# Optimization experiments

Hardware: AMD Instinct MI355X
Metric: run time of the kernel (lower is better)

Reference implementation:

```python
import jax, jax.numpy as jnp
import numpy as np

N = 8192      # n_nodes (graphs[0].shape[0])
E = 262144    # n_edges (avg degree 32)
B = 16        # batch
T = 15        # time taps H of ChebTimeConv
K = 25        # Chebyshev order
G1, G2 = 32, 64
C, D = 512, 6


def setup_inputs() -> dict:
    key = jax.random.key(0)
    ks = jax.random.split(key, 8)
    x = jax.random.normal(ks[0], (B, N, T), jnp.float32)
    edge_index = jax.random.randint(ks[1], (2, E), 0, N, dtype=jnp.int64)
    # ChebTimeConv weights: K Chebyshev taps x T time taps (f_in=1) -> G1
    W1 = jax.random.normal(ks[2], (K, T, G1), jnp.float32) * 0.05
    b1 = jnp.zeros((G1,), jnp.float32)
    # ChebConv weights: K taps, G1 -> G2
    W2 = jax.random.normal(ks[3], (K, G1, G2), jnp.float32) * 0.05
    b2 = jnp.zeros((G2,), jnp.float32)
    fc1_w = jax.random.normal(ks[4], (C, N * G2), jnp.float32) * 0.01
    fc1_b = jnp.zeros((C,), jnp.float32)
    fc2_w = jax.random.normal(ks[5], (D, C), jnp.float32) * 0.05
    fc2_b = jnp.zeros((D,), jnp.float32)
    return dict(x=x, edge_index=edge_index, W1=W1, b1=b1, W2=W2, b2=b2,
                fc1_w=fc1_w, fc1_b=fc1_b, fc2_w=fc2_w, fc2_b=fc2_b)


def _cheb_edge_norm(edge_index, n):
    # PyG ChebConv normalization with lambda_max=2:
    # L_hat = 2L/lambda_max - I = -D^{-1/2} A D^{-1/2} (diag cancels to 0)
    row, col = edge_index[0], edge_index[1]
    deg = jnp.zeros((n,), jnp.float32).at[row].add(1.0)
    dinv = jnp.where(deg > 0, jax.lax.rsqrt(jnp.maximum(deg, 1.0)), 0.0)
    return -(dinv[row] * dinv[col])


def _cheb_conv(x, edge_index, W, b):
    # x: [B, N, Fin]; W: [K, Fin, Fout] -> [B, N, Fout]
    row, col = edge_index[0], edge_index[1]
    norm = _cheb_edge_norm(edge_index, x.shape[1])

    def Lhat(z):  # sparse L_hat @ z : gather at source row, scatter-add at col
        msg = z[:, row, :] * norm[None, :, None]
        return jnp.zeros_like(z).at[:, col, :].add(msg)

    Tx0 = x
    out = jnp.einsum('bnf,fg->bng', Tx0, W[0])
    Tx1 = Lhat(x)
    out = out + jnp.einsum('bnf,fg->bng', Tx1, W[1])
    for k in range(2, W.shape[0]):  # fixed small K=25 recursion
        Tx2 = 2.0 * Lhat(Tx1) - Tx0
        out = out + jnp.einsum('bnf,fg->bng', Tx2, W[k])
        Tx0, Tx1 = Tx1, Tx2
    return out + b


def reference(x, edge_index, W1, b1, W2, b2, fc1_w, fc1_b, fc2_w, fc2_b):
    # torch: real part of FFT over the time axis
    xf = jnp.fft.fft(x, axis=2).real.astype(x.dtype)          # [B, N, T]
    h = jax.nn.relu(_cheb_conv(xf, edge_index, W1, b1))       # [B, N, G1]
    h = jax.nn.relu(_cheb_conv(h, edge_index, W2, b2))        # [B, N, G2]
    h = h.reshape(h.shape[0], -1)                             # [B, N*G2]
    h = h @ fc1_w.T + fc1_b                                   # [B, C]
    h = h @ fc2_w.T + fc2_b                                   # [B, D]
    return jax.nn.log_softmax(h, axis=1)
```

## Files before the change

kernel.cpp:

```cpp
#include <hip/hip_runtime.h>
#include <hip/hip_bf16.h>

typedef _Float16 f16x2 __attribute__((ext_vector_type(2)));
typedef _Float16 f16x4 __attribute__((ext_vector_type(4)));
typedef _Float16 f16x8 __attribute__((ext_vector_type(8)));
typedef float f32x4 __attribute__((ext_vector_type(4)));

static constexpr int NNODE = 8192;
static constexpr int NEDGE = 262144;
static constexpr int NBATCH = 16;
static constexpr int TDIM = 15;
static constexpr int G1D = 32;
static constexpr int G2D = 64;
static constexpr int NK = 25;
static constexpr size_t NG2 = (size_t)NNODE * G2D;
static constexpr size_t ROWDW = 128;
static constexpr size_t SLICE = (size_t)NNODE * ROWDW;


__global__ void deg_cnt_kernel(const int* __restrict__ ei, int* __restrict__ deg,
                               int* __restrict__ cnt) {
    int e = blockIdx.x * 256 + threadIdx.x;
    if (e < NEDGE) {
        atomicAdd(&deg[ei[e]], 1);
        atomicAdd(&cnt[ei[NEDGE + e]], 1);
    }
}

__global__ void dinv_kernel(const int* __restrict__ deg, float* __restrict__ dinv) {
    int n = blockIdx.x * 256 + threadIdx.x;
    if (n < NNODE) dinv[n] = (deg[n] > 0) ? rsqrtf((float)deg[n]) : 0.f;
}

__global__ __launch_bounds__(1024) void scan_kernel(const int* __restrict__ cnt,
                                                    int* __restrict__ ptr) {
    __shared__ int s[1024];
    int t = threadIdx.x;
    int base = t * 8;
    int loc[8];
    int sum = 0;
#pragma unroll
    for (int i = 0; i < 8; ++i) { loc[i] = sum; sum += cnt[base + i]; }
    s[t] = sum;
    __syncthreads();
    for (int off = 1; off < 1024; off <<= 1) {
        int v = (t >= off) ? s[t - off] : 0;
        __syncthreads();
        s[t] += v;
        __syncthreads();
    }
    int prev = (t > 0) ? s[t - 1] : 0;
#pragma unroll
    for (int i = 0; i < 8; ++i) ptr[base + i] = prev + loc[i];
    if (t == 1023) ptr[NNODE] = s[1023];
}

__global__ void fill_kernel(const int* __restrict__ ei, const int* __restrict__ ptr,
                            int* __restrict__ fill, const float* __restrict__ dinv,
                            int* __restrict__ csr_src, float* __restrict__ csr_w) {
    int e = blockIdx.x * 256 + threadIdx.x;
    if (e < NEDGE) {
        int r = ei[e], c = ei[NEDGE + e];
        int pos = ptr[c] + atomicAdd(&fill[c], 1);
        csr_src[pos] = r;
        csr_w[pos] = -dinv[r] * dinv[c];
    }
}


__global__ __launch_bounds__(256) void fft_kernel(const float* __restrict__ x,
                                                  _Float16* __restrict__ T0) {
    int n = blockIdx.x;
    __shared__ float xl[NBATCH][TDIM];
    __shared__ float ct[TDIM][TDIM];
    int t = threadIdx.x;
    if (t < NBATCH * TDIM) {
        int b = t / TDIM, s = t % TDIM;
        xl[b][s] = x[((size_t)b * NNODE + n) * TDIM + s];
    }
    if (t < TDIM * TDIM) {
        int tt = t / TDIM, s = t % TDIM;
        ct[tt][s] = cosf(6.283185307179586f * (float)((tt * s) % TDIM) / 15.0f);
    }
    __syncthreads();
    int b = t >> 4, f = t & 15;
    float a = 0.f;
    if (f < TDIM) {
#pragma unroll
        for (int s = 0; s < TDIM; ++s) a += xl[b][s] * ct[f][s];
    }
    T0[(size_t)n * 256 + t] = (_Float16)a;
}


__global__ void wt_kernel(const float* __restrict__ W, _Float16* __restrict__ Wt,
                          int F, int G, int total) {
    int i = blockIdx.x * 256 + threadIdx.x;
    if (i < total) {
        int f = i & 31;
        int g = (i >> 5) % G;
        int k = i / (32 * G);
        float v = (f < F) ? W[((size_t)k * F + f) * G + g] : 0.f;
        Wt[i] = (_Float16)v;
    }
}


template <bool FIRST>
__global__ __launch_bounds__(128) void gather_step(
    const f16x2* __restrict__ Tsrc, const f16x2* __restrict__ T0,
    f16x2* __restrict__ T2, const int* __restrict__ cptr,
    const int* __restrict__ csrc, const float* __restrict__ cw) {
    __shared__ int es[128];
    __shared__ float ews[128];
    const int c = blockIdx.x;
    const int tid = threadIdx.x;

    float a0 = 0.f, a1 = 0.f;
    const int p0 = cptr[c], p1 = cptr[c + 1];
    for (int tb = p0; tb < p1; tb += 128) {
        int m = p1 - tb;
        if (m > 128) m = 128;
        __syncthreads();
        if (tid < m) { es[tid] = csrc[tb + tid]; ews[tid] = cw[tb + tid]; }
        __syncthreads();
        int j = 0;
        for (; j + 4 <= m; j += 4) {
            int s0 = es[j], s1 = es[j + 1], s2 = es[j + 2], s3 = es[j + 3];
            float w0 = ews[j], w1 = ews[j + 1], w2 = ews[j + 2], w3 = ews[j + 3];
            f16x2 r0 = Tsrc[(size_t)s0 * ROWDW + tid];
            f16x2 r1 = Tsrc[(size_t)s1 * ROWDW + tid];
            f16x2 r2 = Tsrc[(size_t)s2 * ROWDW + tid];
            f16x2 r3 = Tsrc[(size_t)s3 * ROWDW + tid];
            a0 += w0 * (float)r0[0]; a1 += w0 * (float)r0[1];
            a0 += w1 * (float)r1[0]; a1 += w1 * (float)r1[1];
            a0 += w2 * (float)r2[0]; a1 += w2 * (float)r2[1];
            a0 += w3 * (float)r3[0]; a1 += w3 * (float)r3[1];
        }
        for (; j < m; ++j) {
            int s = es[j]; float w = ews[j];
            f16x2 r = Tsrc[(size_t)s * ROWDW + tid];
            a0 += w * (float)r[0]; a1 += w * (float)r[1];
        }
    }

    f16x2 o;
    if (FIRST) {
        o[0] = (_Float16)a0; o[1] = (_Float16)a1;
    } else {
        f16x2 t0v = T0[(size_t)c * ROWDW + tid];
        o[0] = (_Float16)(2.f * a0 - (float)t0v[0]);
        o[1] = (_Float16)(2.f * a1 - (float)t0v[1]);
    }
    T2[(size_t)c * ROWDW + tid] = o;
}


template <int FDW, int G, int MODE>
__global__ __launch_bounds__(G * 4) void proj_kernel(
    const unsigned int* __restrict__ Tall, const _Float16* __restrict__ Wt,
    const float* __restrict__ bias, _Float16* __restrict__ dest) {
    constexpr int STRIDE = NK * 32 + 8;
    constexpr int NT = G * 4;
    __shared__ _Float16 A[16 * STRIDE];
    unsigned int* Adw = reinterpret_cast<unsigned int*>(A);

    const int n = blockIdx.x;
    const int tid = threadIdx.x;

    for (int i = tid; i < 16 * STRIDE / 2; i += NT) Adw[i] = 0u;
    __syncthreads();

    for (int idx = tid; idx < NK * 16 * FDW; idx += NT) {
        int k = idx / (16 * FDW);
        int r = idx % (16 * FDW);
        int b = r / FDW;
        int jp = r % FDW;
        size_t src;
        if (MODE == 0) {
            src = (size_t)k * SLICE + (size_t)n * ROWDW + b * FDW + jp;
        } else {
            src = (size_t)(k * 2 + (b >> 3)) * SLICE + (size_t)n * ROWDW + (b & 7) * FDW + jp;
        }
        Adw[b * (STRIDE / 2) + k * 16 + jp] = Tall[src];
    }
    __syncthreads();

    const int wv = tid >> 6, lane = tid & 63;
    const int m0 = lane & 15;
    const int krow = lane >> 4;
    const int k0 = krow * 8;
    const int g = wv * 16 + m0;

    const float bb = bias[g];
    f32x4 d = (f32x4){bb, bb, bb, bb};
#pragma unroll
    for (int k = 0; k < NK; ++k) {
        f16x8 af = *reinterpret_cast<const f16x8*>(&A[m0 * STRIDE + k * 32 + k0]);
        f16x8 bf = *reinterpret_cast<const f16x8*>(&Wt[((size_t)k * G + g) * 32 + k0]);
        d = __builtin_amdgcn_mfma_f32_16x16x32_f16(af, bf, d, 0, 0, 0);
    }
#pragma unroll
    for (int r = 0; r < 4; ++r) {
        int b = krow * 4 + r;
        _Float16 v = (_Float16)fmaxf(d[r], 0.f);
        if (MODE == 0) {
            dest[((size_t)(b >> 3) * NNODE + n) * 256 + (b & 7) * 32 + g] = v;
        } else {
            dest[(size_t)b * NG2 + (size_t)n * G2D + g] = v;
        }
    }
}


__global__ __launch_bounds__(512) void fc1_kernel(const _Float16* __restrict__ Hflat,
                                                  const float* __restrict__ fc1w,
                                                  float* __restrict__ partial) {
    int wave = threadIdx.x >> 6, lane = threadIdx.x & 63;
    int chunk = blockIdx.x & 127, cg = blockIdx.x >> 7;
    int c0 = (cg * 8 + wave) * 2;
    const float* w0 = fc1w + (size_t)c0 * NG2 + (size_t)chunk * 4096;
    const float* w1 = w0 + NG2;
    const _Float16* h = Hflat + (size_t)chunk * 4096;
    float a0[16], a1[16];
#pragma unroll
    for (int b = 0; b < 16; ++b) { a0[b] = 0.f; a1[b] = 0.f; }
    for (int it = 0; it < 16; ++it) {
        int j = it * 256 + lane * 4;
        float4 wv0 = *reinterpret_cast<const float4*>(w0 + j);
        float4 wv1 = *reinterpret_cast<const float4*>(w1 + j);
#pragma unroll
        for (int b = 0; b < 16; ++b) {
            f16x4 hv = *reinterpret_cast<const f16x4*>(h + (size_t)b * NG2 + j);
            float h0 = (float)hv[0], h1 = (float)hv[1], h2 = (float)hv[2], h3 = (float)hv[3];
            a0[b] += wv0.x * h0 + wv0.y * h1 + wv0.z * h2 + wv0.w * h3;
            a1[b] += wv1.x * h0 + wv1.y * h1 + wv1.z * h2 + wv1.w * h3;
        }
    }
#pragma unroll
    for (int b = 0; b < 16; ++b) {
        float v0 = a0[b], v1 = a1[b];
        for (int off = 32; off; off >>= 1) {
            v0 += __shfl_down(v0, off);
            v1 += __shfl_down(v1, off);
        }
        if (lane == 0) {
            partial[((size_t)chunk * 512 + c0) * 16 + b] = v0;
            partial[((size_t)chunk * 512 + c0 + 1) * 16 + b] = v1;
        }
    }
}

__global__ void fc1_reduce_kernel(const float* __restrict__ partial,
                                  const float* __restrict__ fc1b, float* __restrict__ h1) {
    int i = blockIdx.x * 256 + threadIdx.x;
    if (i < 512 * 16) {
        int b = i & 15, c = i >> 4;
        float s = fc1b[c];
        for (int ch = 0; ch < 128; ++ch) s += partial[((size_t)ch * 512 + c) * 16 + b];
        h1[b * 512 + c] = s;
    }
}

__global__ __launch_bounds__(1024) void fc2_kernel(const float* __restrict__ h1,
                                                   const float* __restrict__ fc2w,
                                                   const float* __restrict__ fc2b,
                                                   float* __restrict__ out) {
    __shared__ float z[16][8];
    int wave = threadIdx.x >> 6, lane = threadIdx.x & 63;
    for (int d = 0; d < 6; ++d) {
        float acc = 0.f;
        for (int c = lane; c < 512; c += 64) acc += h1[wave * 512 + c] * fc2w[d * 512 + c];
        for (int off = 32; off; off >>= 1) acc += __shfl_down(acc, off);
        if (lane == 0) z[wave][d] = acc + fc2b[d];
    }
    __syncthreads();
    int t = threadIdx.x;
    if (t < 96) {
        int b = t / 6, d = t % 6;
        float m = z[b][0];
#pragma unroll
        for (int j = 1; j < 6; ++j) m = fmaxf(m, z[b][j]);
        float se = 0.f;
#pragma unroll
        for (int j = 0; j < 6; ++j) se += expf(z[b][j] - m);
        out[b * 6 + d] = z[b][d] - m - logf(se);
    }
}


extern "C" void kernel_launch(void* const* d_in, const int* in_sizes, int n_in,
                              void* d_out, int out_size, void* d_ws, size_t ws_size,
                              hipStream_t stream) {
    const float* x = (const float*)d_in[0];
    const int* ei = (const int*)d_in[1];
    const float* W1 = (const float*)d_in[2];
    const float* b1 = (const float*)d_in[3];
    const float* W2 = (const float*)d_in[4];
    const float* b2 = (const float*)d_in[5];
    const float* fc1w = (const float*)d_in[6];
    const float* fc1b = (const float*)d_in[7];
    const float* fc2w = (const float*)d_in[8];
    const float* fc2b = (const float*)d_in[9];
    float* out = (float*)d_out;

    char* ws = (char*)d_ws;
    size_t o = 0;
    auto alloc = [&](size_t bytes) -> void* {
        void* p = ws + o;
        o += (bytes + 255) & ~(size_t)255;
        return p;
    };
    f16x2* Tall1 = (f16x2*)alloc(NK * SLICE * 4);
    f16x2* Tall2 = (f16x2*)alloc(NK * 2 * SLICE * 4);
    _Float16* Hflat = (_Float16*)alloc(NBATCH * NG2 * 2);
    float* partial = (float*)alloc((size_t)128 * 512 * 16 * 4);
    int* deg = (int*)alloc(3 * NNODE * 4);
    int* cnt = deg + NNODE;
    int* fill = cnt + NNODE;
    int* cptr = (int*)alloc((NNODE + 8) * 4);
    float* dinv = (float*)alloc(NNODE * 4);
    int* csr_src = (int*)alloc((size_t)NEDGE * 4);
    float* csr_w = (float*)alloc((size_t)NEDGE * 4);
    _Float16* Wt1 = (_Float16*)alloc(NK * G1D * 32 * 2);
    _Float16* Wt2 = (_Float16*)alloc(NK * G2D * 32 * 2);
    float* h1 = (float*)alloc(16 * 512 * 4);

    hipMemsetAsync(deg, 0, 3 * NNODE * 4, stream);
    deg_cnt_kernel<<<NEDGE / 256, 256, 0, stream>>>(ei, deg, cnt);
    dinv_kernel<<<NNODE / 256, 256, 0, stream>>>(deg, dinv);
    scan_kernel<<<1, 1024, 0, stream>>>(cnt, cptr);
    fill_kernel<<<NEDGE / 256, 256, 0, stream>>>(ei, cptr, fill, dinv, csr_src, csr_w);
    fft_kernel<<<NNODE, 256, 0, stream>>>(x, (_Float16*)Tall1);
    wt_kernel<<<(NK * G1D * 32 + 255) / 256, 256, 0, stream>>>(W1, Wt1, 15, G1D,
                                                               NK * G1D * 32);
    wt_kernel<<<(NK * G2D * 32 + 255) / 256, 256, 0, stream>>>(W2, Wt2, 32, G2D,
                                                               NK * G2D * 32);

    gather_step<true><<<NNODE, 128, 0, stream>>>(Tall1, nullptr, Tall1 + SLICE, cptr,
                                                 csr_src, csr_w);
    for (int k = 2; k < NK; ++k) {
        gather_step<false><<<NNODE, 128, 0, stream>>>(
            Tall1 + (size_t)(k - 1) * SLICE, Tall1 + (size_t)(k - 2) * SLICE,
            Tall1 + (size_t)k * SLICE, cptr, csr_src, csr_w);
    }
    proj_kernel<8, G1D, 0><<<NNODE, G1D * 4, 0, stream>>>(
        (const unsigned int*)Tall1, Wt1, b1, (_Float16*)Tall2);

    for (int h = 0; h < 2; ++h) {
        gather_step<true><<<NNODE, 128, 0, stream>>>(
            Tall2 + (size_t)h * SLICE, nullptr, Tall2 + (size_t)(2 + h) * SLICE, cptr,
            csr_src, csr_w);
        for (int k = 2; k < NK; ++k) {
            gather_step<false><<<NNODE, 128, 0, stream>>>(
                Tall2 + (size_t)((k - 1) * 2 + h) * SLICE,
                Tall2 + (size_t)((k - 2) * 2 + h) * SLICE,
                Tall2 + (size_t)(k * 2 + h) * SLICE, cptr, csr_src, csr_w);
        }
    }
    proj_kernel<16, G2D, 1><<<NNODE, G2D * 4, 0, stream>>>(
        (const unsigned int*)Tall2, Wt2, b2, Hflat);

    fc1_kernel<<<128 * 32, 512, 0, stream>>>(Hflat, fc1w, partial);
    fc1_reduce_kernel<<<32, 256, 0, stream>>>(partial, fc1b, h1);
    fc2_kernel<<<1, 1024, 0, stream>>>(h1, fc2w, fc2b, out);
}
```

Baseline: 1.687 ms.

## Split feature slices into 256B rows with XCD-aware wave-per-node gather

Splits each Chebyshev slice into narrower 64-dword sub-slices (two for layer 1, four for layer 2) and remaps block IDs so each XCD handles one sub-slice. That sub-slice's working set can then stay in that XCD's L2 during the gather. Each wave now processes one node, and edge indices and weights are broadcast with readlane instead of shared memory and syncthreads. The second layer's two half-batch loops are merged into one launch per step. The projection kernels are rewritten for the new layout, which adds index-mapping complexity.

```diff
diff --git a/kernel.cpp b/kernel.cpp
--- a/kernel.cpp
+++ b/kernel.cpp
@@ -14,8 +14,8 @@
 static constexpr int G2D = 64;
 static constexpr int NK = 25;
 static constexpr size_t NG2 = (size_t)NNODE * G2D;
-static constexpr size_t ROWDW = 128;
-static constexpr size_t SLICE = (size_t)NNODE * ROWDW;
+static constexpr size_t SROW = 64;
+static constexpr size_t SLICE = (size_t)NNODE * SROW;
 
 
 __global__ void deg_cnt_kernel(const int* __restrict__ ei, int* __restrict__ deg,
@@ -89,7 +89,7 @@
 #pragma unroll
         for (int s = 0; s < TDIM; ++s) a += xl[b][s] * ct[f][s];
     }
-    T0[(size_t)n * 256 + t] = (_Float16)a;
+    T0[((size_t)(b >> 3) * NNODE + n) * 128 + (b & 7) * 16 + f] = (_Float16)a;
 }
 
 
@@ -106,41 +106,52 @@
 }
 
 
-template <bool FIRST>
-__global__ __launch_bounds__(128) void gather_step(
-    const f16x2* __restrict__ Tsrc, const f16x2* __restrict__ T0,
-    f16x2* __restrict__ T2, const int* __restrict__ cptr,
+template <int Q, bool FIRST>
+__global__ __launch_bounds__(256, 8) void gather_step(
+    const f16x2* __restrict__ Tsrc, const f16x2* __restrict__ Tprev0,
+    f16x2* __restrict__ Tdst, const int* __restrict__ cptr,
     const int* __restrict__ csrc, const float* __restrict__ cw) {
-    __shared__ int es[128];
-    __shared__ float ews[128];
-    const int c = blockIdx.x;
-    const int tid = threadIdx.x;
-
+    constexpr int CH = 8 / Q;
+    const int bid = blockIdx.x;
+    const int xcd = bid & 7;
+    const int s = xcd / CH;
+    const int chunk = xcd % CH;
+    const int wv = threadIdx.x >> 6, lane = threadIdx.x & 63;
+    const int node = (chunk * (256 * Q) + (bid >> 3)) * 4 + wv;
+
+    const f16x2* __restrict__ src = Tsrc + (size_t)s * SLICE;
     float a0 = 0.f, a1 = 0.f;
-    const int p0 = cptr[c], p1 = cptr[c + 1];
-    for (int tb = p0; tb < p1; tb += 128) {
+    const int p0 = cptr[node], p1 = cptr[node + 1];
+    for (int tb = p0; tb < p1; tb += 64) {
         int m = p1 - tb;
-        if (m > 128) m = 128;
-        __syncthreads();
-        if (tid < m) { es[tid] = csrc[tb + tid]; ews[tid] = cw[tb + tid]; }
-        __syncthreads();
+        if (m > 64) m = 64;
+        const bool ok = lane < m;
+        int esrc = ok ? csrc[tb + lane] : 0;
+        unsigned int ewu = ok ? __float_as_uint(cw[tb + lane]) : 0u;
         int j = 0;
         for (; j + 4 <= m; j += 4) {
-            int s0 = es[j], s1 = es[j + 1], s2 = es[j + 2], s3 = es[j + 3];
-            float w0 = ews[j], w1 = ews[j + 1], w2 = ews[j + 2], w3 = ews[j + 3];
-            f16x2 r0 = Tsrc[(size_t)s0 * ROWDW + tid];
-            f16x2 r1 = Tsrc[(size_t)s1 * ROWDW + tid];
-            f16x2 r2 = Tsrc[(size_t)s2 * ROWDW + tid];
-            f16x2 r3 = Tsrc[(size_t)s3 * ROWDW + tid];
+            int s0 = __builtin_amdgcn_readlane(esrc, j);
+            int s1 = __builtin_amdgcn_readlane(esrc, j + 1);
+            int s2 = __builtin_amdgcn_readlane(esrc, j + 2);
+            int s3 = __builtin_amdgcn_readlane(esrc, j + 3);
+            float w0 = __uint_as_float(__builtin_amdgcn_readlane(ewu, j));
+            float w1 = __uint_as_float(__builtin_amdgcn_readlane(ewu, j + 1));
+            float w2 = __uint_as_float(__builtin_amdgcn_readlane(ewu, j + 2));
+            float w3 = __uint_as_float(__builtin_amdgcn_readlane(ewu, j + 3));
+            f16x2 r0 = src[(size_t)s0 * SROW + lane];
+            f16x2 r1 = src[(size_t)s1 * SROW + lane];
+            f16x2 r2 = src[(size_t)s2 * SROW + lane];
+            f16x2 r3 = src[(size_t)s3 * SROW + lane];
             a0 += w0 * (float)r0[0]; a1 += w0 * (float)r0[1];
             a0 += w1 * (float)r1[0]; a1 += w1 * (float)r1[1];
             a0 += w2 * (float)r2[0]; a1 += w2 * (float)r2[1];
             a0 += w3 * (float)r3[0]; a1 += w3 * (float)r3[1];
         }
         for (; j < m; ++j) {
-            int s = es[j]; float w = ews[j];
-            f16x2 r = Tsrc[(size_t)s * ROWDW + tid];
-            a0 += w * (float)r[0]; a1 += w * (float)r[1];
+            int sj = __builtin_amdgcn_readlane(esrc, j);
+            float wj = __uint_as_float(__builtin_amdgcn_readlane(ewu, j));
+            f16x2 r = src[(size_t)sj * SROW + lane];
+            a0 += wj * (float)r[0]; a1 += wj * (float)r[1];
         }
     }
 
@@ -148,41 +159,32 @@
     if (FIRST) {
         o[0] = (_Float16)a0; o[1] = (_Float16)a1;
     } else {
-        f16x2 t0v = T0[(size_t)c * ROWDW + tid];
-        o[0] = (_Float16)(2.f * a0 - (float)t0v[0]);
-        o[1] = (_Float16)(2.f * a1 - (float)t0v[1]);
-    }
-    T2[(size_t)c * ROWDW + tid] = o;
-}
-
-
-template <int FDW, int G, int MODE>
-__global__ __launch_bounds__(G * 4) void proj_kernel(
+        f16x2 t0 = (Tprev0 + (size_t)s * SLICE)[(size_t)node * SROW + lane];
+        o[0] = (_Float16)(2.f * a0 - (float)t0[0]);
+        o[1] = (_Float16)(2.f * a1 - (float)t0[1]);
+    }
+    (Tdst + (size_t)s * SLICE)[(size_t)node * SROW + lane] = o;
+}
+
+
+__global__ __launch_bounds__(128) void proj1_kernel(
     const unsigned int* __restrict__ Tall, const _Float16* __restrict__ Wt,
     const float* __restrict__ bias, _Float16* __restrict__ dest) {
     constexpr int STRIDE = NK * 32 + 8;
-    constexpr int NT = G * 4;
     __shared__ _Float16 A[16 * STRIDE];
     unsigned int* Adw = reinterpret_cast<unsigned int*>(A);
-
     const int n = blockIdx.x;
     const int tid = threadIdx.x;
 
-    for (int i = tid; i < 16 * STRIDE / 2; i += NT) Adw[i] = 0u;
-    __syncthreads();
-
-    for (int idx = tid; idx < NK * 16 * FDW; idx += NT) {
-        int k = idx / (16 * FDW);
-        int r = idx % (16 * FDW);
-        int b = r / FDW;
-        int jp = r % FDW;
-        size_t src;
-        if (MODE == 0) {
-            src = (size_t)k * SLICE + (size_t)n * ROWDW + b * FDW + jp;
-        } else {
-            src = (size_t)(k * 2 + (b >> 3)) * SLICE + (size_t)n * ROWDW + (b & 7) * FDW + jp;
-        }
-        Adw[b * (STRIDE / 2) + k * 16 + jp] = Tall[src];
+    for (int i = tid; i < 16 * STRIDE / 2; i += 128) Adw[i] = 0u;
+    __syncthreads();
+    for (int idx = tid; idx < NK * 128; idx += 128) {
+        int k = idx >> 7, r = idx & 127;
+        int h = r >> 6, j = r & 63;
+        int bl = j >> 3, jp = j & 7;
+        int b = h * 8 + bl;
+        Adw[b * (STRIDE / 2) + k * 16 + jp] =
+            Tall[((size_t)(k * 2 + h) * NNODE + n) * 64 + j];
     }
     __syncthreads();
 
@@ -191,24 +193,62 @@
     const int krow = lane >> 4;
     const int k0 = krow * 8;
     const int g = wv * 16 + m0;
-
     const float bb = bias[g];
     f32x4 d = (f32x4){bb, bb, bb, bb};
 #pragma unroll
     for (int k = 0; k < NK; ++k) {
         f16x8 af = *reinterpret_cast<const f16x8*>(&A[m0 * STRIDE + k * 32 + k0]);
-        f16x8 bf = *reinterpret_cast<const f16x8*>(&Wt[((size_t)k * G + g) * 32 + k0]);
+        f16x8 bf = *reinterpret_cast<const f16x8*>(&Wt[((size_t)k * G1D + g) * 32 + k0]);
         d = __builtin_amdgcn_mfma_f32_16x16x32_f16(af, bf, d, 0, 0, 0);
     }
 #pragma unroll
     for (int r = 0; r < 4; ++r) {
         int b = krow * 4 + r;
         _Float16 v = (_Float16)fmaxf(d[r], 0.f);
-        if (MODE == 0) {
-            dest[((size_t)(b >> 3) * NNODE + n) * 256 + (b & 7) * 32 + g] = v;
-        } else {
-            dest[(size_t)b * NG2 + (size_t)n * G2D + g] = v;
-        }
+        dest[((size_t)(b >> 2) * NNODE + n) * 128 + (b & 3) * 32 + g] = v;
+    }
+}
+
+
+__global__ __launch_bounds__(256) void proj2_kernel(
+    const unsigned int* __restrict__ Tall, const _Float16* __restrict__ Wt,
+    const float* __restrict__ bias, _Float16* __restrict__ dest) {
+    constexpr int STRIDE = NK * 32 + 8;
+    __shared__ _Float16 A[16 * STRIDE];
+    unsigned int* Adw = reinterpret_cast<unsigned int*>(A);
+    const int n = blockIdx.x;
+    const int tid = threadIdx.x;
+
+    for (int i = tid; i < 16 * STRIDE / 2; i += 256) Adw[i] = 0u;
+    __syncthreads();
+    for (int idx = tid; idx < NK * 256; idx += 256) {
+        int k = idx >> 8, r = idx & 255;
+        int q = r >> 6, j = r & 63;
+        int bl2 = j >> 4, jp = j & 15;
+        int b = q * 4 + bl2;
+        Adw[b * (STRIDE / 2) + k * 16 + jp] =
+            Tall[((size_t)(k * 4 + q) * NNODE + n) * 64 + j];
+    }
+    __syncthreads();
+
+    const int wv = tid >> 6, lane = tid & 63;
+    const int m0 = lane & 15;
+    const int krow = lane >> 4;
+    const int k0 = krow * 8;
+    const int g = wv * 16 + m0;
+    const float bb = bias[g];
+    f32x4 d = (f32x4){bb, bb, bb, bb};
+#pragma unroll
+    for (int k = 0; k < NK; ++k) {
+        f16x8 af = *reinterpret_cast<const f16x8*>(&A[m0 * STRIDE + k * 32 + k0]);
+        f16x8 bf = *reinterpret_cast<const f16x8*>(&Wt[((size_t)k * G2D + g) * 32 + k0]);
+        d = __builtin_amdgcn_mfma_f32_16x16x32_f16(af, bf, d, 0, 0, 0);
+    }
+#pragma unroll
+    for (int r = 0; r < 4; ++r) {
+        int b = krow * 4 + r;
+        _Float16 v = (_Float16)fmaxf(d[r], 0.f);
+        dest[(size_t)b * NG2 + (size_t)n * G2D + g] = v;
     }
 }
 
@@ -311,8 +351,8 @@
         o += (bytes + 255) & ~(size_t)255;
         return p;
     };
-    f16x2* Tall1 = (f16x2*)alloc(NK * SLICE * 4);
-    f16x2* Tall2 = (f16x2*)alloc(NK * 2 * SLICE * 4);
+    f16x2* Tall1 = (f16x2*)alloc(NK * 2 * SLICE * 4);
+    f16x2* Tall2 = (f16x2*)alloc(NK * 4 * SLICE * 4);
     _Float16* Hflat = (_Float16*)alloc(NBATCH * NG2 * 2);
     float* partial = (float*)alloc((size_t)128 * 512 * 16 * 4);
     int* deg = (int*)alloc(3 * NNODE * 4);
@@ -337,29 +377,24 @@
     wt_kernel<<<(NK * G2D * 32 + 255) / 256, 256, 0, stream>>>(W2, Wt2, 32, G2D,
                                                                NK * G2D * 32);
 
-    gather_step<true><<<NNODE, 128, 0, stream>>>(Tall1, nullptr, Tall1 + SLICE, cptr,
-                                                 csr_src, csr_w);
+    gather_step<2, true><<<4096, 256, 0, stream>>>(Tall1, nullptr, Tall1 + 2 * SLICE,
+                                                   cptr, csr_src, csr_w);
     for (int k = 2; k < NK; ++k) {
-        gather_step<false><<<NNODE, 128, 0, stream>>>(
-            Tall1 + (size_t)(k - 1) * SLICE, Tall1 + (size_t)(k - 2) * SLICE,
-            Tall1 + (size_t)k * SLICE, cptr, csr_src, csr_w);
-    }
-    proj_kernel<8, G1D, 0><<<NNODE, G1D * 4, 0, stream>>>(
-        (const unsigned int*)Tall1, Wt1, b1, (_Float16*)Tall2);
-
-    for (int h = 0; h < 2; ++h) {
-        gather_step<true><<<NNODE, 128, 0, stream>>>(
-            Tall2 + (size_t)h * SLICE, nullptr, Tall2 + (size_t)(2 + h) * SLICE, cptr,
-            csr_src, csr_w);
-        for (int k = 2; k < NK; ++k) {
-            gather_step<false><<<NNODE, 128, 0, stream>>>(
-                Tall2 + (size_t)((k - 1) * 2 + h) * SLICE,
-                Tall2 + (size_t)((k - 2) * 2 + h) * SLICE,
-                Tall2 + (size_t)(k * 2 + h) * SLICE, cptr, csr_src, csr_w);
-        }
-    }
-    proj_kernel<16, G2D, 1><<<NNODE, G2D * 4, 0, stream>>>(
-        (const unsigned int*)Tall2, Wt2, b2, Hflat);
+        gather_step<2, false><<<4096, 256, 0, stream>>>(
+            Tall1 + (size_t)(k - 1) * 2 * SLICE, Tall1 + (size_t)(k - 2) * 2 * SLICE,
+            Tall1 + (size_t)k * 2 * SLICE, cptr, csr_src, csr_w);
+    }
+    proj1_kernel<<<NNODE, 128, 0, stream>>>((const unsigned int*)Tall1, Wt1, b1,
+                                            (_Float16*)Tall2);
+
+    gather_step<4, true><<<8192, 256, 0, stream>>>(Tall2, nullptr, Tall2 + 4 * SLICE,
+                                                   cptr, csr_src, csr_w);
+    for (int k = 2; k < NK; ++k) {
+        gather_step<4, false><<<8192, 256, 0, stream>>>(
+            Tall2 + (size_t)(k - 1) * 4 * SLICE, Tall2 + (size_t)(k - 2) * 4 * SLICE,
+            Tall2 + (size_t)k * 4 * SLICE, cptr, csr_src, csr_w);
+    }
+    proj2_kernel<<<NNODE, 256, 0, stream>>>((const unsigned int*)Tall2, Wt2, b2, Hflat);
 
     fc1_kernel<<<128 * 32, 512, 0, stream>>>(Hflat, fc1w, partial);
     fc1_reduce_kernel<<<32, 256, 0, stream>>>(partial, fc1b, h1);
```

After: 1.529 ms. 1.1x faster.
